# Optimization experiments

Measured on AMD Instinct MI355X. Metric: run time of the kernel, lower is better.

Reference implementation:

```python
import jax, jax.numpy as jnp
import numpy as np

NTIPS = 128   # taxa
NSITES = 1024 # unique site patterns
BS = 32       # batch of trees


def _make_pairs(ntips, bs, seed=0):
    """Valid postorder child/parent triples for random caterpillar trees.

    Mirrors Parsimony._score's child_parent_pairs: [ntips-1, bs, 3], where the
    last step's torch parent=-1 is rewritten to the last state slot 2*ntips-2.
    """
    rng = np.random.default_rng(seed)
    N = 2 * ntips - 1
    pairs = np.zeros((ntips - 1, bs, 3), dtype=np.int32)
    for b in range(bs):
        leaves = rng.permutation(ntips)
        pairs[0, b] = [leaves[0], leaves[1], ntips]
        for i in range(1, ntips - 3):
            pairs[i, b] = [ntips + i - 1, leaves[i + 1], ntips + i]
        root = 2 * ntips - 3
        pairs[ntips - 3, b] = [2 * ntips - 4, leaves[ntips - 2], root]
        pairs[ntips - 2, b] = [root, leaves[ntips - 1], N - 1]
    return pairs


def setup_inputs() -> dict:
    key = jax.random.key(0)
    k1, k2 = jax.random.split(key)
    # one-hot nucleotide states over 5 symbols (A,G,C,T,-)
    nuc = jax.random.randint(k1, (NTIPS, NSITES), 0, 4)
    L = jax.nn.one_hot(nuc, 5, dtype=jnp.int32).transpose(0, 2, 1)  # [ntips,5,S]
    site_counts = jax.random.randint(k2, (NSITES,), 1, 100).astype(jnp.int32)
    pairs = jnp.asarray(_make_pairs(NTIPS, BS))  # [ntips-1, bs, 3]
    return {"L": L, "site_counts": site_counts, "pairs": pairs}


def reference(L, site_counts, pairs):
    ntips, _, S = L.shape
    steps, bs, _ = pairs.shape
    N = 2 * ntips - 1
    base = jnp.concatenate(
        [L, jnp.zeros((N - ntips, 5, S), dtype=L.dtype)], axis=0)  # [N,5,S]
    state0 = jnp.tile(base[None], (bs, 1, 1, 1))   # [bs,N,5,S]
    score0 = jnp.zeros((bs, S), jnp.int32)
    barange = jnp.arange(bs)

    def step(carry, pair):
        state, score = carry
        child, parent = pair[:, :2], pair[:, 2]            # [bs,2], [bs]
        cs = state[barange[:, None], child]                # gather -> [bs,2,5,S]
        inter = cs[:, 0] * cs[:, 1]                        # [bs,5,S]
        union = ((cs[:, 0] + cs[:, 1]) > 0).astype(L.dtype)
        empty = inter.sum(axis=1, keepdims=True) == 0      # [bs,1,S]
        nxt = jnp.where(empty, union, inter)               # Fitch rule
        state = state.at[barange, parent].set(nxt)         # scatter
        score = score + empty[:, 0].astype(jnp.int32)
        return (state, score), None

    (_, score), _ = jax.lax.scan(step, (state0, score0), pairs)
    return jnp.sum(score * site_counts[None, :], axis=-1)  # [bs]
```

## Files before the change

### kernel.cpp

```cpp
#include <hip/hip_runtime.h>
#include <stdint.h>

#define NTIPS 128
#define NSITES 1024
#define BS 32
#define STEPS 127
#define SB 64

__global__ __launch_bounds__(256) void pack_leaves(const int* __restrict__ L,
                                                   uint8_t* __restrict__ packed) {
    int i = blockIdx.x * 256 + threadIdx.x;
    int tip = i >> 10, site = i & 1023;
    const int* b = L + tip * 5 * NSITES + site;
    int m = b[0] | (b[NSITES] << 1) | (b[2 * NSITES] << 2) |
            (b[3 * NSITES] << 3) | (b[4 * NSITES] << 4);
    packed[i] = (uint8_t)m;
}

__global__ __launch_bounds__(64) void fitch_kernel(const int* __restrict__ L,
                                                   const int* __restrict__ site_counts,
                                                   const int* __restrict__ pairs,
                                                   const uint8_t* __restrict__ packed,
                                                   int use_packed,
                                                   int* __restrict__ out) {
    __shared__ int     leafm[NTIPS][SB];
    __shared__ uint8_t internal[STEPS][SB];
    __shared__ int     spairs[STEPS * 3];

    const int tid      = threadIdx.x;
    const int batch    = blockIdx.x >> 4;
    const int siteBase = (blockIdx.x & 15) * SB;
    const int site     = siteBase + tid;

    for (int i = tid; i < STEPS * 3; i += 64) {
        int s = i / 3, j = i - s * 3;
        spairs[i] = pairs[s * (BS * 3) + batch * 3 + j];
    }

    if (use_packed) {
        for (int i = tid; i < NTIPS * (SB / 4); i += 64) {
            int tip = i >> 4, j = i & 15;
            unsigned d = ((const unsigned*)(packed + (tip << 10) + siteBase))[j];
            int4 v = make_int4(d & 255, (d >> 8) & 255, (d >> 16) & 255, (d >> 24) & 255);
            *(int4*)&leafm[tip][j * 4] = v;
        }
    } else {
        for (int tip = 0; tip < NTIPS; ++tip) {
            const int* b = L + tip * 5 * NSITES + site;
            leafm[tip][tid] = b[0] | (b[NSITES] << 1) | (b[2 * NSITES] << 2) |
                              (b[3 * NSITES] << 3) | (b[4 * NSITES] << 4);
        }
    }
    __syncthreads();

    int lastP = -1;
    int lastV = 0;
    int score = 0;
    for (int s = 0; s < STEPS; ++s) {
        int c0 = __builtin_amdgcn_readfirstlane(spairs[3 * s]);
        int c1 = __builtin_amdgcn_readfirstlane(spairs[3 * s + 1]);
        int p  = __builtin_amdgcn_readfirstlane(spairs[3 * s + 2]);
        int m0, m1;
        if (c0 == lastP)     m0 = lastV;
        else if (c0 < NTIPS) m0 = leafm[c0][tid];
        else                 m0 = (int)internal[c0 - NTIPS][tid];
        if (c1 == lastP)     m1 = lastV;
        else if (c1 < NTIPS) m1 = leafm[c1][tid];
        else                 m1 = (int)internal[c1 - NTIPS][tid];
        int inter = m0 & m1;
        int nxt   = inter ? inter : (m0 | m1);
        score    += (inter == 0);
        internal[p - NTIPS][tid] = (uint8_t)nxt;
        lastP = p;
        lastV = nxt;
    }

    int val = score * site_counts[site];
    #pragma unroll
    for (int off = 32; off; off >>= 1) val += __shfl_down(val, off);
    if (tid == 0) atomicAdd(&out[batch], val);
}

extern "C" void kernel_launch(void* const* d_in, const int* in_sizes, int n_in,
                              void* d_out, int out_size, void* d_ws, size_t ws_size,
                              hipStream_t stream) {
    const int* L           = (const int*)d_in[0];
    const int* site_counts = (const int*)d_in[1];
    const int* pairs       = (const int*)d_in[2];
    int* out               = (int*)d_out;

    hipMemsetAsync(out, 0, BS * sizeof(int), stream);

    const size_t packed_bytes = (size_t)NTIPS * NSITES;
    int use_packed = (ws_size >= packed_bytes) ? 1 : 0;
    uint8_t* packed = (uint8_t*)d_ws;

    if (use_packed) {
        pack_leaves<<<dim3((NTIPS * NSITES) / 256), dim3(256), 0, stream>>>(L, packed);
    }
    fitch_kernel<<<dim3(BS * (NSITES / SB)), dim3(64), 0, stream>>>(
        L, site_counts, pairs, packed, use_packed, out);
}
```

Before: 86.53 us.

## Specialize Fitch kernel for caterpillar chains with one block per tree

Replaces the pack kernel and the 512-block shared-memory kernel with a single launch of 32 blocks of 1024 threads, one block per tree. At runtime it checks whether each tree is a chain (each step consumes the previous parent plus a leaf). If so, it carries the running state in a register and reads leaf masks straight from L. Otherwise it falls back to per-tree global workspace. It also drops the memset and atomics by writing each block's sum directly, at the cost of far fewer blocks and uncached, dependent global loads inside the serial loop.

Measured after the change: 82.38 us. 1.05x faster.

```diff
diff --git a/kernel.cpp b/kernel.cpp
--- a/kernel.cpp
+++ b/kernel.cpp
@@ -5,80 +5,91 @@
 #define NSITES 1024
 #define BS 32
 #define STEPS 127
-#define SB 64
+#define NINTERNAL 127
 
-__global__ __launch_bounds__(256) void pack_leaves(const int* __restrict__ L,
-                                                   uint8_t* __restrict__ packed) {
-    int i = blockIdx.x * 256 + threadIdx.x;
-    int tip = i >> 10, site = i & 1023;
-    const int* b = L + tip * 5 * NSITES + site;
-    int m = b[0] | (b[NSITES] << 1) | (b[2 * NSITES] << 2) |
-            (b[3 * NSITES] << 3) | (b[4 * NSITES] << 4);
-    packed[i] = (uint8_t)m;
-}
+__global__ __launch_bounds__(1024) void fitch_kernel(
+    const int* __restrict__ L,
+    const int* __restrict__ site_counts,
+    const int* __restrict__ pairs,
+    uint8_t* __restrict__ ws,
+    int* __restrict__ out)
+{
+    __shared__ int spairs[STEPS * 3];
+    __shared__ int wsum[16];
+    __shared__ int allvalid;
 
-__global__ __launch_bounds__(64) void fitch_kernel(const int* __restrict__ L,
-                                                   const int* __restrict__ site_counts,
-                                                   const int* __restrict__ pairs,
-                                                   const uint8_t* __restrict__ packed,
-                                                   int use_packed,
-                                                   int* __restrict__ out) {
-    __shared__ int     leafm[NTIPS][SB];
-    __shared__ uint8_t internal[STEPS][SB];
-    __shared__ int     spairs[STEPS * 3];
+    const int tid  = threadIdx.x;
+    const int b    = blockIdx.x;
+    const int site = tid;
 
-    const int tid      = threadIdx.x;
-    const int batch    = blockIdx.x >> 4;
-    const int siteBase = (blockIdx.x & 15) * SB;
-    const int site     = siteBase + tid;
-
-    for (int i = tid; i < STEPS * 3; i += 64) {
-        int s = i / 3, j = i - s * 3;
-        spairs[i] = pairs[s * (BS * 3) + batch * 3 + j];
-    }
-
-    if (use_packed) {
-        for (int i = tid; i < NTIPS * (SB / 4); i += 64) {
-            int tip = i >> 4, j = i & 15;
-            unsigned d = ((const unsigned*)(packed + (tip << 10) + siteBase))[j];
-            int4 v = make_int4(d & 255, (d >> 8) & 255, (d >> 16) & 255, (d >> 24) & 255);
-            *(int4*)&leafm[tip][j * 4] = v;
-        }
-    } else {
-        for (int tip = 0; tip < NTIPS; ++tip) {
-            const int* b = L + tip * 5 * NSITES + site;
-            leafm[tip][tid] = b[0] | (b[NSITES] << 1) | (b[2 * NSITES] << 2) |
-                              (b[3 * NSITES] << 3) | (b[4 * NSITES] << 4);
-        }
+    if (tid == 0) allvalid = 1;
+    if (tid < STEPS * 3) {
+        int s = tid / 3, j = tid - s * 3;
+        spairs[tid] = pairs[s * (BS * 3) + b * 3 + j];
     }
     __syncthreads();
 
-    int lastP = -1;
-    int lastV = 0;
+    if (tid < STEPS) {
+        int c0 = spairs[3 * tid], c1 = spairs[3 * tid + 1], p = spairs[3 * tid + 2];
+        bool v = (c1 >= 0) && (c1 < NTIPS) && (p >= NTIPS) &&
+                 (tid == 0 ? (c0 >= 0 && c0 < NTIPS)
+                           : (c0 == spairs[3 * (tid - 1) + 2]));
+        if (!v) allvalid = 0;
+    }
+    __syncthreads();
+
+    const int* Lp = L + site;
     int score = 0;
-    for (int s = 0; s < STEPS; ++s) {
-        int c0 = __builtin_amdgcn_readfirstlane(spairs[3 * s]);
-        int c1 = __builtin_amdgcn_readfirstlane(spairs[3 * s + 1]);
-        int p  = __builtin_amdgcn_readfirstlane(spairs[3 * s + 2]);
-        int m0, m1;
-        if (c0 == lastP)     m0 = lastV;
-        else if (c0 < NTIPS) m0 = leafm[c0][tid];
-        else                 m0 = (int)internal[c0 - NTIPS][tid];
-        if (c1 == lastP)     m1 = lastV;
-        else if (c1 < NTIPS) m1 = leafm[c1][tid];
-        else                 m1 = (int)internal[c1 - NTIPS][tid];
-        int inter = m0 & m1;
-        int nxt   = inter ? inter : (m0 | m1);
-        score    += (inter == 0);
-        internal[p - NTIPS][tid] = (uint8_t)nxt;
-        lastP = p;
-        lastV = nxt;
+
+    #define LEAFMASK(q) ((q)[0] | ((q)[NSITES] << 1) | ((q)[2 * NSITES] << 2) | \
+                         ((q)[3 * NSITES] << 3) | ((q)[4 * NSITES] << 4))
+
+    if (allvalid) {
+        int c00 = __builtin_amdgcn_readfirstlane(spairs[0]);
+        const int* q0 = Lp + c00 * 5 * NSITES;
+        int cur = LEAFMASK(q0);
+        #pragma unroll 8
+        for (int s = 0; s < STEPS; ++s) {
+            int c1 = __builtin_amdgcn_readfirstlane(spairs[3 * s + 1]);
+            const int* q = Lp + c1 * 5 * NSITES;
+            int m1 = LEAFMASK(q);
+            int inter = cur & m1;
+            score += (inter == 0);
+            cur = inter ? inter : (cur | m1);
+        }
+    } else {
+        uint8_t* st = ws + (size_t)b * NINTERNAL * NSITES;
+        int lastP = -1, lastV = 0;
+        for (int s = 0; s < STEPS; ++s) {
+            int c0 = __builtin_amdgcn_readfirstlane(spairs[3 * s]);
+            int c1 = __builtin_amdgcn_readfirstlane(spairs[3 * s + 1]);
+            int p  = __builtin_amdgcn_readfirstlane(spairs[3 * s + 2]);
+            int m0, m1;
+            if (c0 == lastP)        m0 = lastV;
+            else if (c0 < NTIPS)  { const int* q = Lp + c0 * 5 * NSITES; m0 = LEAFMASK(q); }
+            else                    m0 = st[(c0 - NTIPS) * NSITES + site];
+            if (c1 == lastP)        m1 = lastV;
+            else if (c1 < NTIPS)  { const int* q = Lp + c1 * 5 * NSITES; m1 = LEAFMASK(q); }
+            else                    m1 = st[(c1 - NTIPS) * NSITES + site];
+            int inter = m0 & m1;
+            int nxt   = inter ? inter : (m0 | m1);
+            score    += (inter == 0);
+            st[(p - NTIPS) * NSITES + site] = (uint8_t)nxt;
+            lastP = p; lastV = nxt;
+        }
     }
 
     int val = score * site_counts[site];
     #pragma unroll
     for (int off = 32; off; off >>= 1) val += __shfl_down(val, off);
-    if (tid == 0) atomicAdd(&out[batch], val);
+    if ((tid & 63) == 0) wsum[tid >> 6] = val;
+    __syncthreads();
+    if (tid == 0) {
+        int t = 0;
+        #pragma unroll
+        for (int i = 0; i < 16; ++i) t += wsum[i];
+        out[b] = t;
+    }
 }
 
 extern "C" void kernel_launch(void* const* d_in, const int* in_sizes, int n_in,
@@ -87,17 +98,6 @@
     const int* L           = (const int*)d_in[0];
     const int* site_counts = (const int*)d_in[1];
     const int* pairs       = (const int*)d_in[2];
-    int* out               = (int*)d_out;
-
-    hipMemsetAsync(out, 0, BS * sizeof(int), stream);
-
-    const size_t packed_bytes = (size_t)NTIPS * NSITES;
-    int use_packed = (ws_size >= packed_bytes) ? 1 : 0;
-    uint8_t* packed = (uint8_t*)d_ws;
-
-    if (use_packed) {
-        pack_leaves<<<dim3((NTIPS * NSITES) / 256), dim3(256), 0, stream>>>(L, packed);
-    }
-    fitch_kernel<<<dim3(BS * (NSITES / SB)), dim3(64), 0, stream>>>(
-        L, site_counts, pairs, packed, use_packed, out);
+    fitch_kernel<<<dim3(BS), dim3(1024), 0, stream>>>(
+        L, site_counts, pairs, (uint8_t*)d_ws, (int*)d_out);
 }
```
